# Kernel tuning notes

Hardware: AMD Instinct MI355X
Metric: run time of the kernel (lower is better)

## Reference

```python
import jax, jax.numpy as jnp
import numpy as np

B, T, K = 8192, 512, 12
START_TAG, STOP_TAG = 10, 11  # '[CLS]', '[SEP]' indices in default tag_map


def setup_inputs() -> dict:
    key = jax.random.key(0)
    k1, k2 = jax.random.split(key)
    logits = jax.random.normal(k1, (B, T, K), dtype=jnp.float32)
    transitions = jax.random.normal(k2, (K, K), dtype=jnp.float32)
    # constraints applied in BiLSTMCRF.__init__
    transitions = transitions.at[:, START_TAG].set(-1000.0)
    transitions = transitions.at[STOP_TAG, :].set(-1000.0)
    return {"logits": logits, "transitions": transitions}


def reference(logits, transitions):
    """Batched Viterbi decode, matching BiLSTMCRF.__viterbi_decode.

    logits: [B, T, K] emission scores (output of hidden2tag)
    transitions: [K, K] transitions[i, j] = score of tag i -> tag j
    Returns (scores [B], paths [B, T] int32).
    """
    em = jnp.swapaxes(logits, 0, 1)  # [T, B, K]

    def step(prev, emit_t):
        # prev: [B, K] trellis at t-1; v[b, i, j] = prev[b, i] + trans[i, j]
        v = prev[:, :, None] + transitions[None, :, :]  # [B, K, K]
        best = jnp.max(v, axis=1) + emit_t              # [B, K]
        bp = jnp.argmax(v, axis=1).astype(jnp.int32)    # [B, K]
        return best, bp

    final, bps = jax.lax.scan(step, em[0], em[1:])  # final: [B,K], bps: [T-1,B,K]

    scores = jnp.max(final, axis=-1)                     # [B]
    last = jnp.argmax(final, axis=-1).astype(jnp.int32)  # [B], tag at t = T-1

    def back(nxt, bp_t):
        # bp_t[b, j] = best previous tag given tag j at the next step
        cur = jnp.take_along_axis(bp_t, nxt[:, None], axis=1)[:, 0]
        return cur, cur

    # reverse scan: processes bps[T-2] .. bps[0], outputs tags for t = 0 .. T-2
    _, rest = jax.lax.scan(back, last, bps, reverse=True)  # [T-1, B]
    paths = jnp.concatenate([rest, last[None, :]], axis=0)  # [T, B]
    return scores, jnp.swapaxes(paths, 0, 1)
```

## Files before the change

kernel.cpp:

```cpp
#include <hip/hip_runtime.h>
#include <stdint.h>


namespace {

constexpr int kB = 8192;
constexpr int kT = 512;
constexpr int kK = 12;
constexpr int kRows = 4;
constexpr int kRowF = 392;

template <int I>
__device__ __forceinline__ float bcast16(float x) {
    return __int_as_float(__builtin_amdgcn_ds_swizzle(
        __float_as_int(x), (I << 5) | 0x10));
}

__global__ __launch_bounds__(64, 2) void viterbi_fused(
    const float* __restrict__ logits,
    const float* __restrict__ trans,
    float* __restrict__ out,
    uint32_t* __restrict__ bp)
{
    __shared__ float embuf[2][kRows][kRowF];

    const int ln    = threadIdx.x;
    const int grp   = ln >> 4;
    const int jl    = ln & 15;
    const int j     = (jl < 12) ? jl : 11;
    const int brow0 = blockIdx.x * kRows;
    const int b     = brow0 + grp;

    const float T0 = trans[0 * kK + j],  T1 = trans[1 * kK + j];
    const float T2 = trans[2 * kK + j],  T3 = trans[3 * kK + j];
    const float T4 = trans[4 * kK + j],  T5 = trans[5 * kK + j];
    const float T6 = trans[6 * kK + j],  T7 = trans[7 * kK + j];
    const float T8 = trans[8 * kK + j],  T9 = trans[9 * kK + j];
    const float T10 = trans[10 * kK + j], T11 = trans[11 * kK + j];

    uint32_t* __restrict__ bpq = bp + (size_t)b * 1024 + jl;

#define DMA_CHUNK(cc) do {                                                    \
    const int dsel_ = (cc) & 1;                                               \
    _Pragma("unroll")                                                         \
    for (int r_ = 0; r_ < kRows; ++r_) {                                      \
        const float* gs_ = logits + (size_t)(brow0 + r_) * (kT * kK)          \
                           + (cc) * 384 + ln;                                 \
        float* ld_ = &embuf[dsel_][r_][0];                                    \
        _Pragma("unroll")                                                     \
        for (int p_ = 0; p_ < 6; ++p_) {                                      \
            __builtin_amdgcn_global_load_lds(                                 \
                (const __attribute__((address_space(1))) void*)(gs_ + p_ * 64),\
                (__attribute__((address_space(3))) void*)(ld_ + p_ * 64),     \
                4, 0, 0);                                                     \
        }                                                                     \
    }                                                                         \
} while (0)

    auto emrd = [&](int t) -> float {
        const int tc = (t < kT) ? t : (kT - 1);
        return embuf[(tc >> 5) & 1][grp][(tc & 31) * 12 + jl];
    };

    DMA_CHUNK(0);
    DMA_CHUNK(1);

    __builtin_amdgcn_wave_barrier();
    __builtin_amdgcn_s_waitcnt(0x0F70);
    __builtin_amdgcn_wave_barrier();

    float nv = emrd(0);
    uint32_t acc = 0u;

    float e0 = emrd(1), e1 = emrd(2), e2 = emrd(3), e3 = emrd(4);
    float e4 = emrd(5), e5 = emrd(6), e6 = emrd(7), e7 = emrd(8);

#define STEP(TT, EV) do {                                                     \
    const float p0 = bcast16<0>(nv),  p1 = bcast16<1>(nv);                    \
    const float p2 = bcast16<2>(nv),  p3 = bcast16<3>(nv);                    \
    const float p4 = bcast16<4>(nv),  p5 = bcast16<5>(nv);                    \
    const float p6 = bcast16<6>(nv),  p7 = bcast16<7>(nv);                    \
    const float p8 = bcast16<8>(nv),  p9 = bcast16<9>(nv);                    \
    const float p10 = bcast16<10>(nv), p11 = bcast16<11>(nv);                 \
    const float x0 = p0 + T0,  x1 = p1 + T1,  x2 = p2 + T2;                   \
    const float x3 = p3 + T3,  x4 = p4 + T4,  x5 = p5 + T5;                   \
    const float x6 = p6 + T6,  x7 = p7 + T7,  x8 = p8 + T8;                   \
    const float x9 = p9 + T9,  x10 = p10 + T10, x11 = p11 + T11;              \
    const float mA = fmaxf(fmaxf(x0, x1), x2);                                \
    const float mB = fmaxf(fmaxf(x3, x4), x5);                                \
    const float mC = fmaxf(fmaxf(x6, x7), x8);                                \
    const float mD = fmaxf(fmaxf(x9, x10), x11);                              \
    const float best = fmaxf(fmaxf(mA, mB), fmaxf(mC, mD));                   \
    int gA = (x1 == mA) ? 1 : 2;    gA = (x0 == mA) ? 0 : gA;                 \
    int gB = (x4 == mB) ? 4 : 5;    gB = (x3 == mB) ? 3 : gB;                 \
    int gC = (x7 == mC) ? 7 : 8;    gC = (x6 == mC) ? 6 : gC;                 \
    int gD = (x10 == mD) ? 10 : 11; gD = (x9 == mD) ? 9 : gD;                 \
    int bi = gD;                                                              \
    bi = (mC == best) ? gC : bi;                                              \
    bi = (mB == best) ? gB : bi;                                              \
    bi = (mA == best) ? gA : bi;                                              \
    nv = best + (EV);                                                         \
    acc |= (uint32_t)bi << (4 * (((TT) - 1) & 7));                            \
} while (0)

#pragma unroll 1
    for (int sb = 0; sb < 63; ++sb) {
        const int tb = 8 * sb + 1;

        if ((sb & 3) == 2) {
            __builtin_amdgcn_wave_barrier();
            __builtin_amdgcn_s_waitcnt(0x0F70);
            __builtin_amdgcn_wave_barrier();
        }
        if ((sb & 3) == 3) {
            const int cc = (sb >> 2) + 2;
            if (cc <= 15) {
                __builtin_amdgcn_wave_barrier();
                __builtin_amdgcn_s_waitcnt(0xC07F);
                DMA_CHUNK(cc);
                __builtin_amdgcn_wave_barrier();
            }
        }

        const float f0 = emrd(tb + 8),  f1 = emrd(tb + 9);
        const float f2 = emrd(tb + 10), f3 = emrd(tb + 11);
        const float f4 = emrd(tb + 12), f5 = emrd(tb + 13);
        const float f6 = emrd(tb + 14), f7 = emrd(tb + 15);

        STEP(tb + 0, e0); STEP(tb + 1, e1); STEP(tb + 2, e2); STEP(tb + 3, e3);
        STEP(tb + 4, e4); STEP(tb + 5, e5); STEP(tb + 6, e6); STEP(tb + 7, e7);

        bpq[sb * 16] = acc;
        acc = 0u;

        e0 = f0; e1 = f1; e2 = f2; e3 = f3;
        e4 = f4; e5 = f5; e6 = f6; e7 = f7;
    }

    STEP(505, e0); STEP(506, e1); STEP(507, e2); STEP(508, e3);
    STEP(509, e4); STEP(510, e5); STEP(511, e6);
    bpq[63 * 16] = acc;

#undef STEP
#undef DMA_CHUNK

    float best;
    int last;
    {
        const float p0 = bcast16<0>(nv),  p1 = bcast16<1>(nv);
        const float p2 = bcast16<2>(nv),  p3 = bcast16<3>(nv);
        const float p4 = bcast16<4>(nv),  p5 = bcast16<5>(nv);
        const float p6 = bcast16<6>(nv),  p7 = bcast16<7>(nv);
        const float p8 = bcast16<8>(nv),  p9 = bcast16<9>(nv);
        const float p10 = bcast16<10>(nv), p11 = bcast16<11>(nv);
        const float mA = fmaxf(fmaxf(p0, p1), p2);
        const float mB = fmaxf(fmaxf(p3, p4), p5);
        const float mC = fmaxf(fmaxf(p6, p7), p8);
        const float mD = fmaxf(fmaxf(p9, p10), p11);
        best = fmaxf(fmaxf(mA, mB), fmaxf(mC, mD));
        int gA = (p1 == mA) ? 1 : 2;    gA = (p0 == mA) ? 0 : gA;
        int gB = (p4 == mB) ? 4 : 5;    gB = (p3 == mB) ? 3 : gB;
        int gC = (p7 == mC) ? 7 : 8;    gC = (p6 == mC) ? 6 : gC;
        int gD = (p10 == mD) ? 10 : 11; gD = (p9 == mD) ? 9 : gD;
        int bi = gD;
        bi = (mC == best) ? gC : bi;
        bi = (mB == best) ? gB : bi;
        bi = (mA == best) ? gA : bi;
        last = bi;
    }

    __syncthreads();

#define BTS(SUB, PB) do {                                                     \
    const uint32_t e0_ = (tag & 1) ? qa.y : qa.x;                             \
    const uint32_t e1_ = (tag & 1) ? qa.w : qa.z;                             \
    const uint32_t e2_ = (tag & 1) ? qb.y : qb.x;                             \
    const uint32_t e3_ = (tag & 1) ? qb.w : qb.z;                             \
    const uint32_t e4_ = (tag & 1) ? qc.y : qc.x;                             \
    const uint32_t e5_ = (tag & 1) ? qc.w : qc.z;                             \
    const uint32_t f0_ = (tag & 2) ? e1_ : e0_;                               \
    const uint32_t f1_ = (tag & 2) ? e3_ : e2_;                               \
    const uint32_t f2_ = (tag & 2) ? e5_ : e4_;                               \
    const uint32_t g0_ = (tag & 4) ? f1_ : f0_;                               \
    const uint32_t dw_ = (tag >= 8) ? f2_ : g0_;                              \
    tag = (int)((dw_ >> (4 * (SUB))) & 0xFu);                                 \
    paths[(PB) + (SUB)] = (float)tag;                                         \
} while (0)

    if (jl == 0) {
        out[b] = best;
        float* __restrict__ paths = out + kB + (size_t)b * kT;
        paths[kT - 1] = (float)last;

        int tag = last;
        const uint4* __restrict__ rec = (const uint4*)(bp + (size_t)b * 1024);

        uint4 qa = rec[63 * 4 + 0], qb = rec[63 * 4 + 1], qc = rec[63 * 4 + 2];
        uint4 na = rec[62 * 4 + 0], nb = rec[62 * 4 + 1], nc = rec[62 * 4 + 2];

        BTS(6, 504); BTS(5, 504); BTS(4, 504); BTS(3, 504);
        BTS(2, 504); BTS(1, 504); BTS(0, 504);

#pragma unroll 1
        for (int blk = 62; blk >= 0; --blk) {
            qa = na; qb = nb; qc = nc;
            if (blk > 0) {
                na = rec[blk * 4 - 4];
                nb = rec[blk * 4 - 3];
                nc = rec[blk * 4 - 2];
            }
            const int pb = blk * 8;
            BTS(7, pb); BTS(6, pb); BTS(5, pb); BTS(4, pb);
            BTS(3, pb); BTS(2, pb); BTS(1, pb); BTS(0, pb);
        }
    }
#undef BTS
}

}

extern "C" void kernel_launch(void* const* d_in, const int* in_sizes, int n_in,
                              void* d_out, int out_size, void* d_ws, size_t ws_size,
                              hipStream_t stream) {
    const float* logits = (const float*)d_in[0];
    const float* trans  = (const float*)d_in[1];
    float* out = (float*)d_out;
    uint32_t* bp = (uint32_t*)d_ws;

    const int threads = 64;
    const int blocks = kB / kRows;
    viterbi_fused<<<blocks, threads, 0, stream>>>(logits, trans, out, bp);
}
```

Measured before the change: 491.6 us.

## Replace LDS DMA staging of emissions with direct global loads and flat argmax

Drops the double-buffered global_load_lds staging of emission chunks and its waitcnt/barrier schedule, and instead loads each emission value straight from global memory into registers eight steps ahead. The argmax is also rewritten from a two-level group compare into a flat chain of equality selects against the overall max. This removes LDS traffic and explicit synchronisation, but each lane now issues strided 4-byte global loads (stride 48 bytes), so latency hiding depends on the eight-step register prefetch and on the cache. The flat select chain has a longer serial dependency than the grouped version.

```diff
diff --git a/kernel.cpp b/kernel.cpp
--- a/kernel.cpp
+++ b/kernel.cpp
@@ -8,7 +8,6 @@
 constexpr int kT = 512;
 constexpr int kK = 12;
 constexpr int kRows = 4;
-constexpr int kRowF = 392;
 
 template <int I>
 __device__ __forceinline__ float bcast16(float x) {
@@ -22,8 +21,6 @@
     float* __restrict__ out,
     uint32_t* __restrict__ bp)
 {
-    __shared__ float embuf[2][kRows][kRowF];
-
     const int ln    = threadIdx.x;
     const int grp   = ln >> 4;
     const int jl    = ln & 15;
@@ -40,42 +37,20 @@
 
     uint32_t* __restrict__ bpq = bp + (size_t)b * 1024 + jl;
 
-#define DMA_CHUNK(cc) do {                                                    \
-    const int dsel_ = (cc) & 1;                                               \
-    _Pragma("unroll")                                                         \
-    for (int r_ = 0; r_ < kRows; ++r_) {                                      \
-        const float* gs_ = logits + (size_t)(brow0 + r_) * (kT * kK)          \
-                           + (cc) * 384 + ln;                                 \
-        float* ld_ = &embuf[dsel_][r_][0];                                    \
-        _Pragma("unroll")                                                     \
-        for (int p_ = 0; p_ < 6; ++p_) {                                      \
-            __builtin_amdgcn_global_load_lds(                                 \
-                (const __attribute__((address_space(1))) void*)(gs_ + p_ * 64),\
-                (__attribute__((address_space(3))) void*)(ld_ + p_ * 64),     \
-                4, 0, 0);                                                     \
-        }                                                                     \
-    }                                                                         \
-} while (0)
+    const float* __restrict__ gem = logits + (size_t)b * (kT * kK) + j;
 
-    auto emrd = [&](int t) -> float {
+    auto ld = [&](int t) -> float {
         const int tc = (t < kT) ? t : (kT - 1);
-        return embuf[(tc >> 5) & 1][grp][(tc & 31) * 12 + jl];
+        return gem[tc * kK];
     };
 
-    DMA_CHUNK(0);
-    DMA_CHUNK(1);
-
-    __builtin_amdgcn_wave_barrier();
-    __builtin_amdgcn_s_waitcnt(0x0F70);
-    __builtin_amdgcn_wave_barrier();
-
-    float nv = emrd(0);
+    float nv = ld(0);
     uint32_t acc = 0u;
 
-    float e0 = emrd(1), e1 = emrd(2), e2 = emrd(3), e3 = emrd(4);
-    float e4 = emrd(5), e5 = emrd(6), e6 = emrd(7), e7 = emrd(8);
+    float e0 = ld(1), e1 = ld(2), e2 = ld(3), e3 = ld(4);
+    float e4 = ld(5), e5 = ld(6), e6 = ld(7), e7 = ld(8);
 
-#define STEP(TT, EV) do {                                                     \
+#define STEP(TSTEP, EV_) do {                                                 \
     const float p0 = bcast16<0>(nv),  p1 = bcast16<1>(nv);                    \
     const float p2 = bcast16<2>(nv),  p3 = bcast16<3>(nv);                    \
     const float p4 = bcast16<4>(nv),  p5 = bcast16<5>(nv);                    \
@@ -91,41 +66,25 @@
     const float mC = fmaxf(fmaxf(x6, x7), x8);                                \
     const float mD = fmaxf(fmaxf(x9, x10), x11);                              \
     const float best = fmaxf(fmaxf(mA, mB), fmaxf(mC, mD));                   \
-    int gA = (x1 == mA) ? 1 : 2;    gA = (x0 == mA) ? 0 : gA;                 \
-    int gB = (x4 == mB) ? 4 : 5;    gB = (x3 == mB) ? 3 : gB;                 \
-    int gC = (x7 == mC) ? 7 : 8;    gC = (x6 == mC) ? 6 : gC;                 \
-    int gD = (x10 == mD) ? 10 : 11; gD = (x9 == mD) ? 9 : gD;                 \
-    int bi = gD;                                                              \
-    bi = (mC == best) ? gC : bi;                                              \
-    bi = (mB == best) ? gB : bi;                                              \
-    bi = (mA == best) ? gA : bi;                                              \
-    nv = best + (EV);                                                         \
-    acc |= (uint32_t)bi << (4 * (((TT) - 1) & 7));                            \
+    int bi = 11;                                                              \
+    bi = (x10 == best) ? 10 : bi;  bi = (x9 == best) ? 9 : bi;                \
+    bi = (x8  == best) ?  8 : bi;  bi = (x7 == best) ? 7 : bi;                \
+    bi = (x6  == best) ?  6 : bi;  bi = (x5 == best) ? 5 : bi;                \
+    bi = (x4  == best) ?  4 : bi;  bi = (x3 == best) ? 3 : bi;                \
+    bi = (x2  == best) ?  2 : bi;  bi = (x1 == best) ? 1 : bi;                \
+    bi = (x0  == best) ?  0 : bi;                                             \
+    nv = best + (EV_);                                                        \
+    acc |= (uint32_t)bi << (4 * (((TSTEP) - 1) & 7));                         \
 } while (0)
 
 #pragma unroll 1
     for (int sb = 0; sb < 63; ++sb) {
         const int tb = 8 * sb + 1;
 
-        if ((sb & 3) == 2) {
-            __builtin_amdgcn_wave_barrier();
-            __builtin_amdgcn_s_waitcnt(0x0F70);
-            __builtin_amdgcn_wave_barrier();
-        }
-        if ((sb & 3) == 3) {
-            const int cc = (sb >> 2) + 2;
-            if (cc <= 15) {
-                __builtin_amdgcn_wave_barrier();
-                __builtin_amdgcn_s_waitcnt(0xC07F);
-                DMA_CHUNK(cc);
-                __builtin_amdgcn_wave_barrier();
-            }
-        }
-
-        const float f0 = emrd(tb + 8),  f1 = emrd(tb + 9);
-        const float f2 = emrd(tb + 10), f3 = emrd(tb + 11);
-        const float f4 = emrd(tb + 12), f5 = emrd(tb + 13);
-        const float f6 = emrd(tb + 14), f7 = emrd(tb + 15);
+        const float f0 = ld(tb + 8),  f1 = ld(tb + 9);
+        const float f2 = ld(tb + 10), f3 = ld(tb + 11);
+        const float f4 = ld(tb + 12), f5 = ld(tb + 13);
+        const float f6 = ld(tb + 14), f7 = ld(tb + 15);
 
         STEP(tb + 0, e0); STEP(tb + 1, e1); STEP(tb + 2, e2); STEP(tb + 3, e3);
         STEP(tb + 4, e4); STEP(tb + 5, e5); STEP(tb + 6, e6); STEP(tb + 7, e7);
@@ -142,7 +101,6 @@
     bpq[63 * 16] = acc;
 
 #undef STEP
-#undef DMA_CHUNK
 
     float best;
     int last;
@@ -158,14 +116,13 @@
         const float mC = fmaxf(fmaxf(p6, p7), p8);
         const float mD = fmaxf(fmaxf(p9, p10), p11);
         best = fmaxf(fmaxf(mA, mB), fmaxf(mC, mD));
-        int gA = (p1 == mA) ? 1 : 2;    gA = (p0 == mA) ? 0 : gA;
-        int gB = (p4 == mB) ? 4 : 5;    gB = (p3 == mB) ? 3 : gB;
-        int gC = (p7 == mC) ? 7 : 8;    gC = (p6 == mC) ? 6 : gC;
-        int gD = (p10 == mD) ? 10 : 11; gD = (p9 == mD) ? 9 : gD;
-        int bi = gD;
-        bi = (mC == best) ? gC : bi;
-        bi = (mB == best) ? gB : bi;
-        bi = (mA == best) ? gA : bi;
+        int bi = 11;
+        bi = (p10 == best) ? 10 : bi;  bi = (p9 == best) ? 9 : bi;
+        bi = (p8  == best) ?  8 : bi;  bi = (p7 == best) ? 7 : bi;
+        bi = (p6  == best) ?  6 : bi;  bi = (p5 == best) ? 5 : bi;
+        bi = (p4  == best) ?  4 : bi;  bi = (p3 == best) ? 3 : bi;
+        bi = (p2  == best) ?  2 : bi;  bi = (p1 == best) ? 1 : bi;
+        bi = (p0  == best) ?  0 : bi;
         last = bi;
     }
 
```

Result: faster. 445.5 us (-9.4%).
